# Kernel optimization log

Hardware: AMD Instinct MI355X
Metric: run time of the kernel (lower is better)

The kernel has to match this reference:

```python
import jax, jax.numpy as jnp
import numpy as np

TOP_K = 2  # routing_method: renormalize top-2 (topk then softmax over selected logits)


def setup_inputs() -> dict:
    key = jax.random.key(0)
    ks = jax.random.split(key, 5)
    T, H, I, E = 4096, 1024, 4096, 8
    return {
        "hidden_states": jax.random.normal(ks[0], (T, H), jnp.float32),
        "router_logits": jax.random.normal(ks[1], (T, E), jnp.float32),
        "W_gate": jax.random.normal(ks[2], (E, H, I), jnp.float32) * 0.02,  # w1
        "W_up": jax.random.normal(ks[3], (E, H, I), jnp.float32) * 0.02,   # w3
        "W_down": jax.random.normal(ks[4], (E, I, H), jnp.float32) * 0.02, # w2
    }


def reference(hidden_states, router_logits, W_gate, W_up, W_down):
    # Routing: top-k logits, renormalize with softmax over selected logits.
    top_vals, top_idx = jax.lax.top_k(router_logits, TOP_K)        # [T, K]
    routing_weights = jax.nn.softmax(top_vals, axis=-1)            # [T, K]

    E = W_gate.shape[0]
    out = jnp.zeros_like(hidden_states)                            # [T, H]
    for e in range(E):  # fixed small expert loop (structurally distinct weights)
        # combine weight for expert e per token (0 if not routed here)
        w_e = jnp.sum(jnp.where(top_idx == e, routing_weights, 0.0), axis=-1)  # [T]
        gate = hidden_states @ W_gate[e]                           # [T, I]
        up = hidden_states @ W_up[e]                               # [T, I]
        y = (jax.nn.silu(gate) * up) @ W_down[e]                   # [T, H]
        out = out + w_e[:, None] * y
    return out
```

## Files before the change

### kernel.cpp

```cpp
#include <hip/hip_runtime.h>

typedef float    f32x4 __attribute__((ext_vector_type(4)));
typedef _Float16 f16x8 __attribute__((ext_vector_type(8)));
typedef _Float16 f16x4 __attribute__((ext_vector_type(4)));

#define T_TOK 4096
#define HD    1024
#define ID    4096
#define NE    8
#define TOTP  (2*T_TOK)
#define MAXT1 72
#define MAXT2 40

#define WS_CNT   0
#define WS_FILL  64
#define WS_OFF   128
#define WS_TOT   192
#define WS_TOT2  196
#define WS_TEXP  256
#define WS_TM0   (256 + 4*MAXT1)
#define WS_TEXP2 (256 + 8*MAXT1)
#define WS_TM02  (256 + 8*MAXT1 + 4*MAXT2)
#define WS_TOPE  2048
#define WS_TOPW  (WS_TOPE + 4*TOTP)
#define WS_PAIR  (WS_TOPW + 4*TOTP)
#define WS_ACT   ((size_t)1 << 20)
constexpr size_t WS_YBUF = WS_ACT  + 2ull*TOTP*ID;
constexpr size_t WS_HS16 = WS_YBUF + 2ull*TOTP*HD;
constexpr size_t WS_WG16 = WS_HS16 + 2ull*T_TOK*HD;
constexpr size_t WS_WU16 = WS_WG16 + 2ull*NE*HD*ID;
constexpr size_t WS_WD16 = WS_WU16 + 2ull*NE*HD*ID;

__device__ __forceinline__ void gll16(const void* g, void* l) {
  __builtin_amdgcn_global_load_lds(
      (const __attribute__((address_space(1))) unsigned int*)g,
      (__attribute__((address_space(3))) unsigned int*)l, 16, 0, 0);
}

#define WAITV(N) do { \
    asm volatile("s_waitcnt vmcnt(" #N ")" ::: "memory"); \
    __builtin_amdgcn_sched_barrier(0); \
  } while (0)

__device__ __forceinline__ int lofs(int row, int g) {
  return row * 32 + ((g ^ ((row >> 1) & 3)) << 3);
}

__global__ void k_router(const float* __restrict__ logits, char* __restrict__ ws) {
  int t = blockIdx.x * blockDim.x + threadIdx.x;
  if (t >= T_TOK) return;
  float v0 = -1e30f, v1 = -1e30f; int i0 = 0, i1 = 0;
  #pragma unroll
  for (int e = 0; e < NE; ++e) {
    float v = logits[t * NE + e];
    if (v > v0)      { v1 = v0; i1 = i0; v0 = v; i0 = e; }
    else if (v > v1) { v1 = v;  i1 = e; }
  }
  float w0 = 1.f / (1.f + __expf(v1 - v0));
  ((int*)(ws + WS_TOPE))[2*t]   = i0;
  ((int*)(ws + WS_TOPE))[2*t+1] = i1;
  ((float*)(ws + WS_TOPW))[2*t]   = w0;
  ((float*)(ws + WS_TOPW))[2*t+1] = 1.f - w0;
  atomicAdd(&((int*)(ws + WS_CNT))[i0], 1);
  atomicAdd(&((int*)(ws + WS_CNT))[i1], 1);
}

__global__ void k_prefix(char* __restrict__ ws) {
  if (threadIdx.x != 0 || blockIdx.x != 0) return;
  const int* cnt = (const int*)(ws + WS_CNT);
  int* off   = (int*)(ws + WS_OFF);
  int* texp  = (int*)(ws + WS_TEXP);
  int* tm0   = (int*)(ws + WS_TM0);
  int* texp2 = (int*)(ws + WS_TEXP2);
  int* tm02  = (int*)(ws + WS_TM02);
  int run = 0, t1 = 0, t2 = 0;
  for (int e = 0; e < NE; ++e) {
    off[e] = run;
    int ne = cnt[e];
    for (int i = 0; i < ne; i += 128) { texp[t1] = e; tm0[t1] = i; ++t1; }
    for (int i = 0; i < ne; i += 256) { texp2[t2] = e; tm02[t2] = i; ++t2; }
    run += ne;
  }
  off[NE] = run;
  *(int*)(ws + WS_TOT)  = t1;
  *(int*)(ws + WS_TOT2) = t2;
}

__global__ void k_scatter(char* __restrict__ ws) {
  int t = blockIdx.x * blockDim.x + threadIdx.x;
  if (t >= T_TOK) return;
  const int* tope = (const int*)(ws + WS_TOPE);
  const int* off  = (const int*)(ws + WS_OFF);
  int* fill = (int*)(ws + WS_FILL);
  int* pair = (int*)(ws + WS_PAIR);
  #pragma unroll
  for (int s = 0; s < 2; ++s) {
    int id = 2*t + s;
    int e = tope[id];
    int pos = off[e] + atomicAdd(&fill[e], 1);
    pair[pos] = id;
  }
}

__global__ void k_hscvt(const float* __restrict__ src, _Float16* __restrict__ dst) {
  int i = blockIdx.x * blockDim.x + threadIdx.x;
  f32x4 v = ((const f32x4*)src)[i];
  f16x4 o;
  #pragma unroll
  for (int j = 0; j < 4; ++j) o[j] = (_Float16)v[j];
  ((f16x4*)dst)[i] = o;
}

__global__ __launch_bounds__(256) void k_wtrans(const float* __restrict__ src,
                                                _Float16* __restrict__ dst,
                                                int K, int N) {
  const int e = blockIdx.z;
  const int n0 = blockIdx.x * 64, k0 = blockIdx.y * 64;
  const float* s = src + (size_t)e * K * N;
  _Float16* d = dst + (size_t)e * (size_t)K * N;
  __shared__ _Float16 t[64][68];
  const int tx = threadIdx.x & 15, ty = threadIdx.x >> 4;
  #pragma unroll
  for (int it = 0; it < 4; ++it) {
    int k = k0 + it*16 + ty;
    f32x4 v = *(const f32x4*)&s[(size_t)k * N + n0 + tx*4];
    #pragma unroll
    for (int j = 0; j < 4; ++j) t[tx*4 + j][it*16 + ty] = (_Float16)v[j];
  }
  __syncthreads();
  #pragma unroll
  for (int it = 0; it < 4; ++it) {
    int n = it*16 + ty;
    *(f16x4*)&d[(size_t)(n0 + n) * K + k0 + tx*4] = *(const f16x4*)&t[n][tx*4];
  }
}

#define G1_BUF 20480
__global__ __launch_bounds__(512) void k_gemm1(
    const _Float16* __restrict__ hs16, const _Float16* __restrict__ WgT,
    const _Float16* __restrict__ WuT, char* __restrict__ ws) {
  const int s = blockIdx.y;
  if (s >= *(const int*)(ws + WS_TOT)) return;
  const int e    = ((const int*)(ws + WS_TEXP))[s];
  const int m0   = ((const int*)(ws + WS_TM0))[s];
  const int offE = ((const int*)(ws + WS_OFF))[e];
  const int nE   = ((const int*)(ws + WS_CNT))[e];
  _Float16* __restrict__ act = (_Float16*)(ws + WS_ACT);
  const int n0 = blockIdx.x * 256;
  const int tid = threadIdx.x, lane = tid & 63, wid = tid >> 6;

  __shared__ __align__(16) _Float16 sm[3 * G1_BUF];

  const int rL = lane >> 2;
  const int q  = (((lane & 3) ^ ((lane >> 3) & 3)) << 3);
  int tok;
  { int mm = m0 + 16*wid + rL;
    tok = (mm < nE) ? (((const int*)(ws + WS_PAIR))[offE + mm] >> 1) : 0; }
  const _Float16* aS  = hs16 + (size_t)tok * HD + q;
  const size_t cB0 = (size_t)e * ID + n0 + 32*wid + rL;
  const _Float16* gS0 = WgT + cB0 * HD + q;
  const _Float16* gS1 = gS0 + 16ull * HD;
  const _Float16* uS0 = WuT + cB0 * HD + q;
  const _Float16* uS1 = uS0 + 16ull * HD;

  auto stageAG = [&](int buf, int kt) {
    _Float16* b = sm + buf * G1_BUF;
    const int ko = kt * 32;
    gll16(aS  + ko, b + wid*512);
    gll16(gS0 + ko, b + 4096  + wid*1024);
    gll16(gS1 + ko, b + 4096  + wid*1024 + 512);
  };
  auto stageU = [&](int buf, int kt) {
    _Float16* b = sm + buf * G1_BUF;
    const int ko = kt * 32;
    gll16(uS0 + ko, b + 12288 + wid*1024);
    gll16(uS1 + ko, b + 12288 + wid*1024 + 512);
  };

  const int wr = wid >> 2, wc = wid & 3;
  const int l15 = lane & 15, l4 = lane >> 4;
  f32x4 accg[4][4] = {}, accu[4][4] = {};

  auto compute = [&](int buf) {
    const _Float16* b0 = sm + buf * G1_BUF;
    f16x8 afr[4], bfr[4];
    #pragma unroll
    for (int i = 0; i < 4; ++i)
      afr[i] = *(const f16x8*)&b0[lofs(64*wr + 16*i + l15, l4)];
    #pragma unroll
    for (int j = 0; j < 4; ++j)
      bfr[j] = *(const f16x8*)&b0[4096 + lofs(64*wc + 16*j + l15, l4)];
    __builtin_amdgcn_s_setprio(1);
    #pragma unroll
    for (int i = 0; i < 4; ++i)
      #pragma unroll
      for (int j = 0; j < 4; ++j)
        accg[i][j] = __builtin_amdgcn_mfma_f32_16x16x32_f16(afr[i], bfr[j], accg[i][j], 0, 0, 0);
    __builtin_amdgcn_s_setprio(0);
    #pragma unroll
    for (int j = 0; j < 4; ++j)
      bfr[j] = *(const f16x8*)&b0[12288 + lofs(64*wc + 16*j + l15, l4)];
    __builtin_amdgcn_s_setprio(1);
    #pragma unroll
    for (int i = 0; i < 4; ++i)
      #pragma unroll
      for (int j = 0; j < 4; ++j)
        accu[i][j] = __builtin_amdgcn_mfma_f32_16x16x32_f16(afr[i], bfr[j], accu[i][j], 0, 0, 0);
    __builtin_amdgcn_s_setprio(0);
  };

  const int KT = HD / 32;
  stageAG(0, 0); stageU(0, 0);
  stageAG(1, 1); stageU(1, 1);
  for (int t = 0; t < KT - 2; ++t) {
    const int nb = (t + 2) % 3;
    stageAG(nb, t + 2);
    WAITV(8);
    __builtin_amdgcn_s_barrier();
    stageU(nb, t + 2);
    compute(t % 3);
    __builtin_amdgcn_s_barrier();
  }
  WAITV(5);
  __builtin_amdgcn_s_barrier();
  compute((KT - 2) % 3);
  __builtin_amdgcn_s_barrier();
  WAITV(0);
  __builtin_amdgcn_s_barrier();
  compute((KT - 1) % 3);

  #pragma unroll
  for (int i = 0; i < 4; ++i)
    #pragma unroll
    for (int r = 0; r < 4; ++r) {
      const int mm = m0 + 64*wr + 16*i + 4*l4 + r;
      if (mm < nE) {
        const size_t prow = (size_t)(offE + mm) * ID;
        #pragma unroll
        for (int j = 0; j < 4; ++j) {
          float g = accg[i][j][r], u = accu[i][j][r];
          float sv = g / (1.f + __expf(-g)) * u;
          act[prow + n0 + 64*wc + 16*j + l15] = (_Float16)sv;
        }
      }
    }
}

#define G2_BUF 12288
__global__ __launch_bounds__(512) void k_gemm2(const _Float16* __restrict__ WdT,
                                               char* __restrict__ ws) {
  const int s = blockIdx.y;
  if (s >= *(const int*)(ws + WS_TOT2)) return;
  const int e    = ((const int*)(ws + WS_TEXP2))[s];
  const int m0   = ((const int*)(ws + WS_TM02))[s];
  const int offE = ((const int*)(ws + WS_OFF))[e];
  const int nE   = ((const int*)(ws + WS_CNT))[e];
  const int* __restrict__ pair = (const int*)(ws + WS_PAIR);
  const _Float16* __restrict__ act = (const _Float16*)(ws + WS_ACT);
  _Float16* __restrict__ ybuf = (_Float16*)(ws + WS_YBUF);
  const int n0 = blockIdx.x * 128;
  const int tid = threadIdx.x, lane = tid & 63, wid = tid >> 6;

  __shared__ __align__(16) _Float16 sm[3 * G2_BUF];

  const int rL = lane >> 2;
  const int q  = (((lane & 3) ^ ((lane >> 3) & 3)) << 3);
  int pA0, pA1;
  { int mm = m0 + 32*wid + rL;       pA0 = (mm < nE) ? (offE + mm) : offE; }
  { int mm = m0 + 32*wid + 16 + rL;  pA1 = (mm < nE) ? (offE + mm) : offE; }
  const _Float16* aS0 = act + (size_t)pA0 * ID + q;
  const _Float16* aS1 = act + (size_t)pA1 * ID + q;
  const _Float16* bS  = WdT + ((size_t)e * HD + n0 + 16*wid + rL) * ID + q;

  auto stageBA = [&](int buf, int kt) {
    _Float16* b = sm + buf * G2_BUF;
    const int ko = kt * 32;
    gll16(bS  + ko, b + 8192 + wid*512);
    gll16(aS0 + ko, b + wid*1024);
  };
  auto stageA1 = [&](int buf, int kt) {
    _Float16* b = sm + buf * G2_BUF;
    gll16(aS1 + kt*32, b + wid*1024 + 512);
  };

  const int wr = wid >> 1, wc = wid & 1;
  const int l15 = lane & 15, l4 = lane >> 4;
  f32x4 acc[4][4] = {};

  auto compute = [&](int buf) {
    const _Float16* b0 = sm + buf * G2_BUF;
    f16x8 afr[4], bfr[4];
    #pragma unroll
    for (int i = 0; i < 4; ++i)
      afr[i] = *(const f16x8*)&b0[lofs(64*wr + 16*i + l15, l4)];
    #pragma unroll
    for (int j = 0; j < 4; ++j)
      bfr[j] = *(const f16x8*)&b0[8192 + lofs(64*wc + 16*j + l15, l4)];
    __builtin_amdgcn_s_setprio(1);
    #pragma unroll
    for (int i = 0; i < 4; ++i)
      #pragma unroll
      for (int j = 0; j < 4; ++j)
        acc[i][j] = __builtin_amdgcn_mfma_f32_16x16x32_f16(afr[i], bfr[j], acc[i][j], 0, 0, 0);
    __builtin_amdgcn_s_setprio(0);
  };

  const int KT = ID / 32;
  stageBA(0, 0); stageA1(0, 0);
  stageBA(1, 1); stageA1(1, 1);
  for (int t = 0; t < KT - 2; ++t) {
    const int nb = (t + 2) % 3;
    stageBA(nb, t + 2);
    WAITV(5);
    __builtin_amdgcn_s_barrier();
    stageA1(nb, t + 2);
    compute(t % 3);
    __builtin_amdgcn_s_barrier();
  }
  WAITV(3);
  __builtin_amdgcn_s_barrier();
  compute((KT - 2) % 3);
  __builtin_amdgcn_s_barrier();
  WAITV(0);
  __builtin_amdgcn_s_barrier();
  compute((KT - 1) % 3);

  #pragma unroll
  for (int i = 0; i < 4; ++i)
    #pragma unroll
    for (int r = 0; r < 4; ++r) {
      const int mm = m0 + 64*wr + 16*i + 4*l4 + r;
      if (mm < nE) {
        const int id = pair[offE + mm];
        #pragma unroll
        for (int j = 0; j < 4; ++j)
          ybuf[(size_t)id * HD + n0 + 64*wc + 16*j + l15] = (_Float16)acc[i][j][r];
      }
    }
}

__global__ void k_combine(const char* __restrict__ ws, float* __restrict__ out) {
  const int idx = blockIdx.x * blockDim.x + threadIdx.x;
  const int t = idx >> 7, c = idx & 127;
  const float* topw = (const float*)(ws + WS_TOPW);
  const _Float16* yb = (const _Float16*)(ws + WS_YBUF);
  f16x8 y0 = ((const f16x8*)(yb + (size_t)(2*t)     * HD))[c];
  f16x8 y1 = ((const f16x8*)(yb + (size_t)(2*t + 1) * HD))[c];
  const float w0 = topw[2*t], w1 = topw[2*t+1];
  f32x4 o0, o1;
  #pragma unroll
  for (int j = 0; j < 4; ++j) {
    o0[j] = w0 * (float)y0[j]     + w1 * (float)y1[j];
    o1[j] = w0 * (float)y0[4 + j] + w1 * (float)y1[4 + j];
  }
  ((f32x4*)out)[2*idx]     = o0;
  ((f32x4*)out)[2*idx + 1] = o1;
}

extern "C" void kernel_launch(void* const* d_in, const int* in_sizes, int n_in,
                              void* d_out, int out_size, void* d_ws, size_t ws_size,
                              hipStream_t stream) {
  const float* hs     = (const float*)d_in[0];
  const float* logits = (const float*)d_in[1];
  const float* Wg     = (const float*)d_in[2];
  const float* Wu     = (const float*)d_in[3];
  const float* Wd     = (const float*)d_in[4];
  char* ws = (char*)d_ws;

  _Float16* hs16 = (_Float16*)(ws + WS_HS16);
  _Float16* wg16 = (_Float16*)(ws + WS_WG16);
  _Float16* wu16 = (_Float16*)(ws + WS_WU16);
  _Float16* wd16 = (_Float16*)(ws + WS_WD16);

  hipMemsetAsync(ws, 0, 256, stream);
  k_router <<<dim3(T_TOK/256), dim3(256), 0, stream>>>(logits, ws);
  k_prefix <<<dim3(1),         dim3(64),  0, stream>>>(ws);
  k_scatter<<<dim3(T_TOK/256), dim3(256), 0, stream>>>(ws);
  k_hscvt  <<<dim3(T_TOK*HD/4/256), dim3(256), 0, stream>>>(hs, hs16);
  k_wtrans <<<dim3(ID/64, HD/64, NE), dim3(256), 0, stream>>>(Wg, wg16, HD, ID);
  k_wtrans <<<dim3(ID/64, HD/64, NE), dim3(256), 0, stream>>>(Wu, wu16, HD, ID);
  k_wtrans <<<dim3(HD/64, ID/64, NE), dim3(256), 0, stream>>>(Wd, wd16, ID, HD);
  k_gemm1  <<<dim3(ID/256, MAXT1), dim3(512), 0, stream>>>(hs16, wg16, wu16, ws);
  k_gemm2  <<<dim3(HD/128, MAXT2), dim3(512), 0, stream>>>(wd16, ws);
  k_combine<<<dim3(T_TOK*HD/8/256), dim3(256), 0, stream>>>(ws, (float*)d_out);
}
```

Before: 533.4 us.

## Shrink GEMM blocks to 256 threads with two blocks per CU and unrolled triple-buffer loop

Both expert GEMMs drop from 512-thread to 256-thread blocks with launch bounds requesting two blocks per CU. gemm1 halves its N tile from 256 to 128 and its shared buffer to match. gemm2 keeps the 128x128 tile but each warp now owns 128 rows, using eight accumulator rows instead of four. The staging is merged into a single batch per step and the main loop is unrolled by three so buffer indices are constants, with wait counts changed to fit. The aim is better latency hiding through co-resident blocks and cheaper loop control, at the cost of more registers per thread in gemm2 and more blocks to schedule for gemm1.

Result: faster. 506.7 us (-5.0%).

```diff
diff --git a/kernel.cpp b/kernel.cpp
--- a/kernel.cpp
+++ b/kernel.cpp
@@ -135,8 +135,8 @@
   }
 }
 
-#define G1_BUF 20480
-__global__ __launch_bounds__(512) void k_gemm1(
+#define G1_BUF 12288
+__global__ __launch_bounds__(256, 2) void k_gemm1(
     const _Float16* __restrict__ hs16, const _Float16* __restrict__ WgT,
     const _Float16* __restrict__ WuT, char* __restrict__ ws) {
   const int s = blockIdx.y;
@@ -146,38 +146,36 @@
   const int offE = ((const int*)(ws + WS_OFF))[e];
   const int nE   = ((const int*)(ws + WS_CNT))[e];
   _Float16* __restrict__ act = (_Float16*)(ws + WS_ACT);
-  const int n0 = blockIdx.x * 256;
+  const int n0 = blockIdx.x * 128;
   const int tid = threadIdx.x, lane = tid & 63, wid = tid >> 6;
 
   __shared__ __align__(16) _Float16 sm[3 * G1_BUF];
 
   const int rL = lane >> 2;
   const int q  = (((lane & 3) ^ ((lane >> 3) & 3)) << 3);
-  int tok;
-  { int mm = m0 + 16*wid + rL;
-    tok = (mm < nE) ? (((const int*)(ws + WS_PAIR))[offE + mm] >> 1) : 0; }
-  const _Float16* aS  = hs16 + (size_t)tok * HD + q;
-  const size_t cB0 = (size_t)e * ID + n0 + 32*wid + rL;
-  const _Float16* gS0 = WgT + cB0 * HD + q;
-  const _Float16* gS1 = gS0 + 16ull * HD;
-  const _Float16* uS0 = WuT + cB0 * HD + q;
-  const _Float16* uS1 = uS0 + 16ull * HD;
-
-  auto stageAG = [&](int buf, int kt) {
-    _Float16* b = sm + buf * G1_BUF;
+  const _Float16 *aS[2], *gS[2], *uS[2];
+  #pragma unroll
+  for (int j = 0; j < 2; ++j) {
+    int mm = m0 + 32*wid + 16*j + rL;
+    int tok = (mm < nE) ? (((const int*)(ws + WS_PAIR))[offE + mm] >> 1) : 0;
+    aS[j] = hs16 + (size_t)tok * HD + q;
+    size_t cB = (size_t)e * ID + (n0 + 32*wid + 16*j + rL);
+    gS[j] = WgT + cB * HD + q;
+    uS[j] = WuT + cB * HD + q;
+  }
+
+  auto stage = [&](int buf, int kt) {
+    _Float16* b = sm + buf * G1_BUF + wid*1024;
     const int ko = kt * 32;
-    gll16(aS  + ko, b + wid*512);
-    gll16(gS0 + ko, b + 4096  + wid*1024);
-    gll16(gS1 + ko, b + 4096  + wid*1024 + 512);
-  };
-  auto stageU = [&](int buf, int kt) {
-    _Float16* b = sm + buf * G1_BUF;
-    const int ko = kt * 32;
-    gll16(uS0 + ko, b + 12288 + wid*1024);
-    gll16(uS1 + ko, b + 12288 + wid*1024 + 512);
-  };
-
-  const int wr = wid >> 2, wc = wid & 3;
+    #pragma unroll
+    for (int j = 0; j < 2; ++j) {
+      gll16(aS[j] + ko, b + j*512);
+      gll16(gS[j] + ko, b + 4096 + j*512);
+      gll16(uS[j] + ko, b + 8192 + j*512);
+    }
+  };
+
+  const int wr = wid >> 1, wc = wid & 1;
   const int l15 = lane & 15, l4 = lane >> 4;
   f32x4 accg[4][4] = {}, accu[4][4] = {};
 
@@ -199,7 +197,7 @@
     __builtin_amdgcn_s_setprio(0);
     #pragma unroll
     for (int j = 0; j < 4; ++j)
-      bfr[j] = *(const f16x8*)&b0[12288 + lofs(64*wc + 16*j + l15, l4)];
+      bfr[j] = *(const f16x8*)&b0[8192 + lofs(64*wc + 16*j + l15, l4)];
     __builtin_amdgcn_s_setprio(1);
     #pragma unroll
     for (int i = 0; i < 4; ++i)
@@ -209,25 +207,28 @@
     __builtin_amdgcn_s_setprio(0);
   };
 
+  auto step = [&](int t, int cur, int nb) {
+    stage(nb, t + 2);
+    WAITV(12);
+    __builtin_amdgcn_s_barrier();
+    compute(cur);
+    __builtin_amdgcn_s_barrier();
+  };
+
   const int KT = HD / 32;
-  stageAG(0, 0); stageU(0, 0);
-  stageAG(1, 1); stageU(1, 1);
-  for (int t = 0; t < KT - 2; ++t) {
-    const int nb = (t + 2) % 3;
-    stageAG(nb, t + 2);
-    WAITV(8);
-    __builtin_amdgcn_s_barrier();
-    stageU(nb, t + 2);
-    compute(t % 3);
-    __builtin_amdgcn_s_barrier();
-  }
-  WAITV(5);
-  __builtin_amdgcn_s_barrier();
-  compute((KT - 2) % 3);
+  stage(0, 0); stage(1, 1);
+  for (int t = 0; t < KT - 2; t += 3) {
+    step(t,     0, 2);
+    step(t + 1, 1, 0);
+    step(t + 2, 2, 1);
+  }
+  WAITV(6);
+  __builtin_amdgcn_s_barrier();
+  compute(0);
   __builtin_amdgcn_s_barrier();
   WAITV(0);
   __builtin_amdgcn_s_barrier();
-  compute((KT - 1) % 3);
+  compute(1);
 
   #pragma unroll
   for (int i = 0; i < 4; ++i)
@@ -247,8 +248,8 @@
 }
 
 #define G2_BUF 12288
-__global__ __launch_bounds__(512) void k_gemm2(const _Float16* __restrict__ WdT,
-                                               char* __restrict__ ws) {
+__global__ __launch_bounds__(256, 2) void k_gemm2(const _Float16* __restrict__ WdT,
+                                                  char* __restrict__ ws) {
   const int s = blockIdx.y;
   if (s >= *(const int*)(ws + WS_TOT2)) return;
   const int e    = ((const int*)(ws + WS_TEXP2))[s];
@@ -265,71 +266,76 @@
 
   const int rL = lane >> 2;
   const int q  = (((lane & 3) ^ ((lane >> 3) & 3)) << 3);
-  int pA0, pA1;
-  { int mm = m0 + 32*wid + rL;       pA0 = (mm < nE) ? (offE + mm) : offE; }
-  { int mm = m0 + 32*wid + 16 + rL;  pA1 = (mm < nE) ? (offE + mm) : offE; }
-  const _Float16* aS0 = act + (size_t)pA0 * ID + q;
-  const _Float16* aS1 = act + (size_t)pA1 * ID + q;
-  const _Float16* bS  = WdT + ((size_t)e * HD + n0 + 16*wid + rL) * ID + q;
-
-  auto stageBA = [&](int buf, int kt) {
+  const _Float16 *aS[4], *bS[2];
+  #pragma unroll
+  for (int j = 0; j < 4; ++j) {
+    int mm = m0 + 64*wid + 16*j + rL;
+    int p = (mm < nE) ? (offE + mm) : offE;
+    aS[j] = act + (size_t)p * ID + q;
+  }
+  #pragma unroll
+  for (int j = 0; j < 2; ++j)
+    bS[j] = WdT + ((size_t)e * HD + (n0 + 32*wid + 16*j + rL)) * ID + q;
+
+  auto stage = [&](int buf, int kt) {
     _Float16* b = sm + buf * G2_BUF;
     const int ko = kt * 32;
-    gll16(bS  + ko, b + 8192 + wid*512);
-    gll16(aS0 + ko, b + wid*1024);
-  };
-  auto stageA1 = [&](int buf, int kt) {
-    _Float16* b = sm + buf * G2_BUF;
-    gll16(aS1 + kt*32, b + wid*1024 + 512);
+    #pragma unroll
+    for (int j = 0; j < 4; ++j) gll16(aS[j] + ko, b + wid*2048 + j*512);
+    #pragma unroll
+    for (int j = 0; j < 2; ++j) gll16(bS[j] + ko, b + 8192 + wid*1024 + j*512);
   };
 
   const int wr = wid >> 1, wc = wid & 1;
   const int l15 = lane & 15, l4 = lane >> 4;
-  f32x4 acc[4][4] = {};
+  f32x4 acc[8][4] = {};
 
   auto compute = [&](int buf) {
     const _Float16* b0 = sm + buf * G2_BUF;
-    f16x8 afr[4], bfr[4];
-    #pragma unroll
-    for (int i = 0; i < 4; ++i)
-      afr[i] = *(const f16x8*)&b0[lofs(64*wr + 16*i + l15, l4)];
+    f16x8 afr[8], bfr[4];
+    #pragma unroll
+    for (int i = 0; i < 8; ++i)
+      afr[i] = *(const f16x8*)&b0[lofs(128*wr + 16*i + l15, l4)];
     #pragma unroll
     for (int j = 0; j < 4; ++j)
       bfr[j] = *(const f16x8*)&b0[8192 + lofs(64*wc + 16*j + l15, l4)];
     __builtin_amdgcn_s_setprio(1);
     #pragma unroll
-    for (int i = 0; i < 4; ++i)
+    for (int i = 0; i < 8; ++i)
       #pragma unroll
       for (int j = 0; j < 4; ++j)
         acc[i][j] = __builtin_amdgcn_mfma_f32_16x16x32_f16(afr[i], bfr[j], acc[i][j], 0, 0, 0);
     __builtin_amdgcn_s_setprio(0);
   };
 
+  auto step = [&](int t, int cur, int nb) {
+    stage(nb, t + 2);
+    WAITV(12);
+    __builtin_amdgcn_s_barrier();
+    compute(cur);
+    __builtin_amdgcn_s_barrier();
+  };
+
   const int KT = ID / 32;
-  stageBA(0, 0); stageA1(0, 0);
-  stageBA(1, 1); stageA1(1, 1);
-  for (int t = 0; t < KT - 2; ++t) {
-    const int nb = (t + 2) % 3;
-    stageBA(nb, t + 2);
-    WAITV(5);
-    __builtin_amdgcn_s_barrier();
-    stageA1(nb, t + 2);
-    compute(t % 3);
-    __builtin_amdgcn_s_barrier();
-  }
-  WAITV(3);
-  __builtin_amdgcn_s_barrier();
-  compute((KT - 2) % 3);
+  stage(0, 0); stage(1, 1);
+  for (int t = 0; t < KT - 2; t += 3) {
+    step(t,     0, 2);
+    step(t + 1, 1, 0);
+    step(t + 2, 2, 1);
+  }
+  WAITV(6);
+  __builtin_amdgcn_s_barrier();
+  compute(0);
   __builtin_amdgcn_s_barrier();
   WAITV(0);
   __builtin_amdgcn_s_barrier();
-  compute((KT - 1) % 3);
-
-  #pragma unroll
-  for (int i = 0; i < 4; ++i)
+  compute(1);
+
+  #pragma unroll
+  for (int i = 0; i < 8; ++i)
     #pragma unroll
     for (int r = 0; r < 4; ++r) {
-      const int mm = m0 + 64*wr + 16*i + 4*l4 + r;
+      const int mm = m0 + 128*wr + 16*i + 4*l4 + r;
       if (mm < nE) {
         const int id = pair[offE + mm];
         #pragma unroll
@@ -380,7 +386,7 @@
   k_wtrans <<<dim3(ID/64, HD/64, NE), dim3(256), 0, stream>>>(Wg, wg16, HD, ID);
   k_wtrans <<<dim3(ID/64, HD/64, NE), dim3(256), 0, stream>>>(Wu, wu16, HD, ID);
   k_wtrans <<<dim3(HD/64, ID/64, NE), dim3(256), 0, stream>>>(Wd, wd16, ID, HD);
-  k_gemm1  <<<dim3(ID/256, MAXT1), dim3(512), 0, stream>>>(hs16, wg16, wu16, ws);
-  k_gemm2  <<<dim3(HD/128, MAXT2), dim3(512), 0, stream>>>(wd16, ws);
+  k_gemm1  <<<dim3(ID/128, MAXT1), dim3(256), 0, stream>>>(hs16, wg16, wu16, ws);
+  k_gemm2  <<<dim3(HD/128, MAXT2), dim3(256), 0, stream>>>(wd16, ws);
   k_combine<<<dim3(T_TOK*HD/8/256), dim3(256), 0, stream>>>(ws, (float*)d_out);
 }
```
